# Performance work log

Measured on AMD Instinct MI355X. Metric: run time of the kernel, lower is better.

The kernel has to match this reference:

```python
import math
import jax, jax.numpy as jnp
import numpy as np

B, C, H, W = 64, 1536, 16, 16
M_CLUSTERS, L_DIM, G_DIM, HID = 64, 128, 256, 512


def setup_inputs() -> dict:
    key = jax.random.key(0)
    ks = jax.random.split(key, 10)

    def w(k, out_d, in_d):
        return jax.random.normal(k, (out_d, in_d), jnp.float32) * (1.0 / np.sqrt(in_d))

    return {
        "x": jax.random.normal(ks[0], (B, C, H, W), jnp.float32),
        "t": jax.random.normal(ks[1], (B, C), jnp.float32),
        # token_features: Linear(C,512) -> ReLU -> Linear(512, token_dim)
        "Wt1": w(ks[2], HID, C), "bt1": jnp.zeros((HID,), jnp.float32),
        "Wt2": w(ks[3], G_DIM, HID), "bt2": jnp.zeros((G_DIM,), jnp.float32),
        # cluster_features: Conv1x1(C,512) -> ReLU -> Conv1x1(512, cluster_dim)
        "Wc1": w(ks[4], HID, C), "bc1": jnp.zeros((HID,), jnp.float32),
        "Wc2": w(ks[5], L_DIM, HID), "bc2": jnp.zeros((L_DIM,), jnp.float32),
        # score: Conv1x1(C,512) -> ReLU -> Conv1x1(512, num_clusters)
        "Ws1": w(ks[6], HID, C), "bs1": jnp.zeros((HID,), jnp.float32),
        "Ws2": w(ks[7], M_CLUSTERS, HID), "bs2": jnp.zeros((M_CLUSTERS,), jnp.float32),
        "dust_bin": jnp.float32(1.0),
    }


def _l2norm(a, axis):
    n = jnp.maximum(jnp.linalg.norm(a, axis=axis, keepdims=True), 1e-12)
    return a / n


def _conv1x1_mlp(xf, W1, b1, W2, b2):
    # xf: [B, C, N]; 1x1 convs are channel GEMMs
    h = jax.nn.relu(jnp.einsum('oc,bcn->bon', W1, xf) + b1[None, :, None])
    return jnp.einsum('oc,bcn->bon', W2, h) + b2[None, :, None]


def _matching_probs(S, dust_bin, num_iters=3):
    # Sinkhorn with dustbin row (log domain), reg = 1.0
    b, m, n = S.shape
    dust_row = jnp.broadcast_to(dust_bin.astype(S.dtype), (b, 1, n))
    Ms = jnp.concatenate([S, dust_row], axis=1)  # [B, m+1, n]
    norm = -math.log(n + m)
    log_a = jnp.full((m + 1,), norm, S.dtype).at[-1].add(math.log(n - m))
    log_b = jnp.full((n,), norm, S.dtype)
    u = jnp.zeros((b, m + 1), S.dtype)
    v = jnp.zeros((b, n), S.dtype)
    for _ in range(num_iters):
        u = log_a[None, :] - jax.scipy.special.logsumexp(Ms + v[:, None, :], axis=2)
        v = log_b[None, :] - jax.scipy.special.logsumexp(Ms + u[:, :, None], axis=1)
    return Ms + u[:, :, None] + v[:, None, :] - norm  # log_P - norm


def reference(x, t, Wt1, bt1, Wt2, bt2, Wc1, bc1, Wc2, bc2, Ws1, bs1, Ws2, bs2, dust_bin):
    b, c, h, w = x.shape
    n = h * w
    xf = x.reshape(b, c, n)
    f = _conv1x1_mlp(xf, Wc1, bc1, Wc2, bc2)      # [B, l, N]
    s = _conv1x1_mlp(xf, Ws1, bs1, Ws2, bs2)      # [B, m, N]
    tok = jax.nn.relu(t @ Wt1.T + bt1) @ Wt2.T + bt2  # [B, g]

    log_p = _matching_probs(s, dust_bin, num_iters=3)
    p = jnp.exp(log_p)[:, :-1, :]                 # drop dustbin row -> [B, m, N]

    # (f.unsqueeze(2) * p.unsqueeze(1)).sum(-1) is exactly a batched matmul
    vlad = jnp.einsum('bln,bmn->blm', f, p)       # [B, l, m]
    vlad = _l2norm(vlad, axis=1).reshape(b, -1)   # intra-norm over l, then flatten(1)

    out = jnp.concatenate([_l2norm(tok, axis=-1), vlad], axis=-1)
    return _l2norm(out, axis=-1)
```

## Files before the change

### kernel.cpp

```cpp
#include <hip/hip_runtime.h>
#include <math.h>

#define BNT 16384

using f32x4 = __attribute__((ext_vector_type(4))) float;
using s16x8 = __attribute__((ext_vector_type(8))) short;

__device__ __forceinline__ unsigned short f32_to_bf16_rne(float f) {
  unsigned int u = __float_as_uint(f);
  u += 0x7FFFu + ((u >> 16) & 1u);
  return (unsigned short)(u >> 16);
}
__device__ __forceinline__ unsigned pack_bf16x2(float a, float b) {
  return (unsigned)f32_to_bf16_rne(a) | ((unsigned)f32_to_bf16_rne(b) << 16);
}

__device__ __forceinline__ void gload_lds16(const ushort* g, ushort* lds) {
  __builtin_amdgcn_global_load_lds(
      (const __attribute__((address_space(1))) unsigned int*)g,
      (__attribute__((address_space(3))) unsigned int*)lds, 16, 0, 0);
}

__global__ __launch_bounds__(256) void prep_all(
    const float* __restrict__ t, const float* __restrict__ Wt1,
    const float* __restrict__ Wt2, const float* __restrict__ Wc1,
    const float* __restrict__ Ws1, const float* __restrict__ bc1,
    const float* __restrict__ bs1, const float* __restrict__ Wc2,
    const float* __restrict__ Ws2, const float* __restrict__ bc2,
    const float* __restrict__ bs2, ushort* __restrict__ Tb,
    ushort* __restrict__ Wt1b, ushort* __restrict__ Wt2b,
    ushort* __restrict__ Wc1b, ushort* __restrict__ Ws1b,
    float* __restrict__ b1, ushort* __restrict__ A2, float* __restrict__ b2) {
  const int bid = blockIdx.x, tid = threadIdx.x;
  const float* src = nullptr;
  ushort* dst = nullptr;
  int i = 0;
  if (bid < 96) {
    src = t; dst = Tb; i = bid * 256 + tid;
  } else if (bid < 864) {
    src = Wt1; dst = Wt1b; i = (bid - 96) * 256 + tid;
  } else if (bid < 992) {
    src = Wt2; dst = Wt2b; i = (bid - 864) * 256 + tid;
  } else if (bid < 1760) {
    src = Wc1; dst = Wc1b; i = (bid - 992) * 256 + tid;
  } else if (bid < 2528) {
    src = Ws1; dst = Ws1b; i = (bid - 1760) * 256 + tid;
  } else if (bid < 2532) {
    const int j = (bid - 2528) * 256 + tid;
    b1[j] = j < 512 ? bc1[j] : bs1[j - 512];
    return;
  } else {
    const int r = bid - 2532;
    const int c = tid * 4;
    float v[4] = {0.f, 0.f, 0.f, 0.f};
    if (r < 128) {
      if (c < 512) {
#pragma unroll
        for (int j = 0; j < 4; ++j) v[j] = Wc2[r * 512 + c + j];
      }
    } else if (r < 192) {
      if (c >= 512) {
#pragma unroll
        for (int j = 0; j < 4; ++j) v[j] = Ws2[(r - 128) * 512 + (c - 512) + j];
      }
    }
    uint2 o;
    o.x = pack_bf16x2(v[0], v[1]);
    o.y = pack_bf16x2(v[2], v[3]);
    *(uint2*)(A2 + r * 1024 + c) = o;
    if (tid == 0) b2[r] = r < 128 ? bc2[r] : (r < 192 ? bs2[r - 128] : 0.f);
    return;
  }
  const float4 v = ((const float4*)src)[i];
  uint2 o;
  o.x = pack_bf16x2(v.x, v.y);
  o.y = pack_bf16x2(v.z, v.w);
  ((uint2*)dst)[i] = o;
}

__global__ __launch_bounds__(256) void token1_mfma(
    const ushort* __restrict__ Tb, const ushort* __restrict__ Wt1b,
    float* __restrict__ Pt) {
  const int ct = blockIdx.x, kc = blockIdx.y;
  const int tid = threadIdx.x, l = tid & 63, wv = tid >> 6;
  const int lr = l & 15, ko = l >> 4;
  const int col = ct * 64 + wv * 16 + lr;
  f32x4 acc[4];
#pragma unroll
  for (int r = 0; r < 4; ++r) acc[r] = (f32x4){0.f, 0.f, 0.f, 0.f};
  const int k0 = kc * 384;
#pragma unroll 4
  for (int ks = 0; ks < 12; ++ks) {
    const int k = k0 + ks * 32 + ko * 8;
    const s16x8 bf = *(const s16x8*)(Wt1b + (size_t)col * 1536 + k);
#pragma unroll
    for (int rf = 0; rf < 4; ++rf) {
      const s16x8 af = *(const s16x8*)(Tb + (size_t)(rf * 16 + lr) * 1536 + k);
      acc[rf] =
          __builtin_amdgcn_mfma_f32_16x16x32_bf16(af, bf, acc[rf], 0, 0, 0);
    }
  }
#pragma unroll
  for (int rf = 0; rf < 4; ++rf)
#pragma unroll
    for (int j = 0; j < 4; ++j) {
      const int row = rf * 16 + ko * 4 + j;
      Pt[((kc * 64 + row) << 9) + col] = acc[rf][j];
    }
}

__global__ __launch_bounds__(256) void token1_reduce(
    const float* __restrict__ Pt, const float* __restrict__ bt1,
    ushort* __restrict__ Hb) {
  const int i = blockIdx.x * 256 + threadIdx.x;
  const int row = i >> 8, c2 = (i & 255) * 2;
  float v0 = bt1[c2], v1 = bt1[c2 + 1];
#pragma unroll
  for (int kc = 0; kc < 4; ++kc) {
    v0 += Pt[((kc * 64 + row) << 9) + c2];
    v1 += Pt[((kc * 64 + row) << 9) + c2 + 1];
  }
  v0 = fmaxf(v0, 0.f);
  v1 = fmaxf(v1, 0.f);
  ((unsigned*)Hb)[i] = pack_bf16x2(v0, v1);
}

__global__ __launch_bounds__(256) void token2_mfma(
    const ushort* __restrict__ Hb, const ushort* __restrict__ Wt2b,
    const float* __restrict__ bt2, float* __restrict__ TK) {
  const int ct = blockIdx.x;
  const int tid = threadIdx.x, l = tid & 63, wv = tid >> 6;
  const int lr = l & 15, ko = l >> 4;
  const int col = ct * 64 + wv * 16 + lr;
  f32x4 acc[4];
#pragma unroll
  for (int r = 0; r < 4; ++r) acc[r] = (f32x4){0.f, 0.f, 0.f, 0.f};
#pragma unroll 4
  for (int ks = 0; ks < 16; ++ks) {
    const int k = ks * 32 + ko * 8;
    const s16x8 bf = *(const s16x8*)(Wt2b + (size_t)col * 512 + k);
#pragma unroll
    for (int rf = 0; rf < 4; ++rf) {
      const s16x8 af = *(const s16x8*)(Hb + (size_t)(rf * 16 + lr) * 512 + k);
      acc[rf] =
          __builtin_amdgcn_mfma_f32_16x16x32_bf16(af, bf, acc[rf], 0, 0, 0);
    }
  }
  const float bb = bt2[col];
#pragma unroll
  for (int rf = 0; rf < 4; ++rf)
#pragma unroll
    for (int j = 0; j < 4; ++j)
      TK[(rf * 16 + ko * 4 + j) * 256 + col] = acc[rf][j] + bb;
}

__global__ __launch_bounds__(256) void transpose_x_bf16(
    const float* __restrict__ x, ushort* __restrict__ XT) {
  __shared__ ushort lds[16384];
  const int cc = blockIdx.x * 64, b = blockIdx.y;
  const int t = threadIdx.x;
  const float* xb = x + b * 393216 + cc * 256;
#pragma unroll
  for (int i = 0; i < 16; ++i) {
    const int c0 = i * 4;
    const float v0 = xb[(c0 + 0) * 256 + t];
    const float v1 = xb[(c0 + 1) * 256 + t];
    const float v2 = xb[(c0 + 2) * 256 + t];
    const float v3 = xb[(c0 + 3) * 256 + t];
    uint2 o;
    o.x = pack_bf16x2(v0, v1);
    o.y = pack_bf16x2(v2, v3);
    const int g = c0 >> 3;
    const int waddr = t * 128 + (((g ^ (t & 7)) << 4) | ((c0 & 7) << 1));
    *(uint2*)((char*)lds + waddr) = o;
  }
  __syncthreads();
#pragma unroll
  for (int r = 0; r < 8; ++r) {
    const int j = r * 32 + (t >> 3), q = t & 7;
    const uint4 o =
        *(const uint4*)((const char*)lds + j * 128 + ((q ^ (j & 7)) << 4));
    *(uint4*)(XT + (size_t)(b * 256 + j) * 1536 + cc + q * 8) = o;
  }
}

__global__ __launch_bounds__(512) void gemm1_win(
    const ushort* __restrict__ A1, const ushort* __restrict__ Bt,
    const float* __restrict__ b1, ushort* __restrict__ HT) {
  __shared__ ushort lds[65536];
  const int tid = threadIdx.x, l = tid & 63, w = tid >> 6;
  const int bid = blockIdx.x;
  const int newid = (bid & 7) * 32 + (bid >> 3);
  const int m0 = (newid & 3) * 256, n0 = (newid >> 2) * 256;
  const int wr = w >> 2, wc = w & 3;
  const int lr = l & 15, kq = l >> 4;
  const int permK8 = (kq ^ ((lr >> 1) & 3)) * 8;
  const int aRow = wr * 128 + lr;
  const int bRow = wc * 64 + lr;

  f32x4 acc[8][4];
#pragma unroll
  for (int mi = 0; mi < 8; ++mi)
#pragma unroll
    for (int ni = 0; ni < 4; ++ni) acc[mi][ni] = (f32x4){0.f, 0.f, 0.f, 0.f};

  const int srow = tid >> 2, ssp = tid & 3;
  const int skq = ssp ^ ((srow >> 1) & 3);
  const ushort* sA0 = A1 + (size_t)(m0 + srow) * 1536 + skq * 8;
  const ushort* sA1 = A1 + (size_t)(m0 + srow + 128) * 1536 + skq * 8;
  const ushort* sB0 = Bt + (size_t)(n0 + srow) * 1536 + skq * 8;
  const ushort* sB1 = Bt + (size_t)(n0 + srow + 128) * 1536 + skq * 8;
  const int wofs = w * 512;

#define STG_A(tau, kh)                                              \
  do {                                                              \
    ushort* d = &lds[((((tau)&1) * 2 + (kh)) * 8192) + wofs];       \
    gload_lds16(sA0 + (tau)*64 + (kh)*32, d);                       \
    gload_lds16(sA1 + (tau)*64 + (kh)*32, d + 4096);                \
  } while (0)
#define STG_B(tau, kh)                                              \
  do {                                                              \
    ushort* d = &lds[32768 + ((((tau)&1) * 2 + (kh)) * 8192) + wofs]; \
    gload_lds16(sB0 + (tau)*64 + (kh)*32, d);                       \
    gload_lds16(sB1 + (tau)*64 + (kh)*32, d + 4096);                \
  } while (0)

  STG_A(0, 0);
  STG_B(0, 0);
  STG_A(0, 1);
  STG_B(0, 1);
  asm volatile("s_waitcnt vmcnt(0)" ::: "memory");
  __builtin_amdgcn_s_barrier();

  for (int sg = 0; sg < 24; ++sg) {
    const int rho = sg & 1;
    const int As0 = (rho * 2 + 0) * 8192, As1 = (rho * 2 + 1) * 8192;
    const int Bs0 = 32768 + As0, Bs1 = 32768 + As1;
    const bool st = (sg + 1) < 24;
    s16x8 af[4], bfv[4];

#pragma unroll
    for (int i = 0; i < 4; ++i)
      af[i] = *(const s16x8*)&lds[As0 + (aRow + i * 16) * 32 + permK8];
#pragma unroll
    for (int ni = 0; ni < 4; ++ni)
      bfv[ni] = *(const s16x8*)&lds[Bs0 + (bRow + ni * 16) * 32 + permK8];
    if (st) STG_A(sg + 1, 0);
#pragma unroll
    for (int i = 0; i < 4; ++i)
#pragma unroll
      for (int ni = 0; ni < 4; ++ni)
        acc[i][ni] = __builtin_amdgcn_mfma_f32_16x16x32_bf16(af[i], bfv[ni],
                                                             acc[i][ni], 0, 0, 0);

#pragma unroll
    for (int i = 0; i < 4; ++i)
      af[i] = *(const s16x8*)&lds[As0 + (aRow + 64 + i * 16) * 32 + permK8];
    if (st) STG_B(sg + 1, 0);
#pragma unroll
    for (int i = 0; i < 4; ++i)
#pragma unroll
      for (int ni = 0; ni < 4; ++ni)
        acc[4 + i][ni] = __builtin_amdgcn_mfma_f32_16x16x32_bf16(
            af[i], bfv[ni], acc[4 + i][ni], 0, 0, 0);

#pragma unroll
    for (int i = 0; i < 4; ++i)
      af[i] = *(const s16x8*)&lds[As1 + (aRow + i * 16) * 32 + permK8];
#pragma unroll
    for (int ni = 0; ni < 4; ++ni)
      bfv[ni] = *(const s16x8*)&lds[Bs1 + (bRow + ni * 16) * 32 + permK8];
    if (st) STG_A(sg + 1, 1);
#pragma unroll
    for (int i = 0; i < 4; ++i)
#pragma unroll
      for (int ni = 0; ni < 4; ++ni)
        acc[i][ni] = __builtin_amdgcn_mfma_f32_16x16x32_bf16(af[i], bfv[ni],
                                                             acc[i][ni], 0, 0, 0);

#pragma unroll
    for (int i = 0; i < 4; ++i)
      af[i] = *(const s16x8*)&lds[As1 + (aRow + 64 + i * 16) * 32 + permK8];
    if (st) STG_B(sg + 1, 1);
#pragma unroll
    for (int i = 0; i < 4; ++i)
#pragma unroll
      for (int ni = 0; ni < 4; ++ni)
        acc[4 + i][ni] = __builtin_amdgcn_mfma_f32_16x16x32_bf16(
            af[i], bfv[ni], acc[4 + i][ni], 0, 0, 0);

    if (st) asm volatile("s_waitcnt vmcnt(0)" ::: "memory");
    __builtin_amdgcn_s_barrier();
  }
#undef STG_A
#undef STG_B

#pragma unroll
  for (int mi = 0; mi < 8; ++mi) {
    const int rbase = m0 + wr * 128 + mi * 16 + kq * 4;
    float b4[4];
#pragma unroll
    for (int j = 0; j < 4; ++j) b4[j] = b1[rbase + j];
#pragma unroll
    for (int ni = 0; ni < 4; ++ni) {
      const int col = n0 + wc * 64 + ni * 16 + lr;
      const float v0 = fmaxf(acc[mi][ni][0] + b4[0], 0.f);
      const float v1 = fmaxf(acc[mi][ni][1] + b4[1], 0.f);
      const float v2 = fmaxf(acc[mi][ni][2] + b4[2], 0.f);
      const float v3 = fmaxf(acc[mi][ni][3] + b4[3], 0.f);
      uint2 o;
      o.x = pack_bf16x2(v0, v1);
      o.y = pack_bf16x2(v2, v3);
      *(uint2*)(HT + (size_t)col * 1024 + rbase) = o;
    }
  }
}

__global__ __launch_bounds__(256) void gemm2_mfma96(
    const ushort* __restrict__ A2, const ushort* __restrict__ HT,
    const float* __restrict__ b2, float* __restrict__ C2,
    ushort* __restrict__ Fb) {
  constexpr int K = 1024;
  __shared__ ushort As[2 * 3072];
  __shared__ ushort Bs[2 * 4096];
  const int tid = threadIdx.x;
  const int l = tid & 63, w = tid >> 6;
  const int bid = blockIdx.x;
  const int newid = (bid & 7) * 32 + (bid >> 3);
  const int m0 = (newid & 1) * 96, n0 = (newid >> 1) * 128;
  const int wr = w >> 1, wc = w & 1;
  const int lr = l & 15, kq = l >> 4;

  f32x4 acc[3][4];
#pragma unroll
  for (int mi = 0; mi < 3; ++mi)
#pragma unroll
    for (int ni = 0; ni < 4; ++ni) acc[mi][ni] = (f32x4){0.f, 0.f, 0.f, 0.f};

  const int srow = tid >> 2;
  const int q8 = (tid & 3) * 8;
  const bool secondA = tid < 128;
  const ushort* sA0 = A2 + (size_t)(m0 + srow) * K + q8;
  const ushort* sA1 = A2 + (size_t)(m0 + srow + 64) * K + q8;
  const ushort* sB0 = HT + (size_t)(n0 + srow) * K + q8;
  const ushort* sB1 = HT + (size_t)(n0 + srow + 64) * K + q8;
  const int wofs = w * 512;

#define STAGE2(k0v, buf)                                            \
  do {                                                              \
    gload_lds16(sA0 + (k0v), As + (buf)*3072 + wofs);               \
    if (secondA) gload_lds16(sA1 + (k0v), As + (buf)*3072 + 2048 + wofs); \
    gload_lds16(sB0 + (k0v), Bs + (buf)*4096 + wofs);               \
    gload_lds16(sB1 + (k0v), Bs + (buf)*4096 + 2048 + wofs);        \
  } while (0)

  STAGE2(0, 0);
  __syncthreads();

  int cur = 0;
  for (int k0 = 0; k0 < K; k0 += 32) {
    const int nxt = cur ^ 1;
    if (k0 + 32 < K) STAGE2(k0 + 32, nxt);
    const ushort* Ab = As + cur * 3072;
    const ushort* Bb = Bs + cur * 4096;
    s16x8 af[3], bfr[4];
#pragma unroll
    for (int mi = 0; mi < 3; ++mi)
      af[mi] = *(const s16x8*)(Ab + (wr * 48 + mi * 16 + lr) * 32 + kq * 8);
#pragma unroll
    for (int ni = 0; ni < 4; ++ni)
      bfr[ni] = *(const s16x8*)(Bb + (wc * 64 + ni * 16 + lr) * 32 + kq * 8);
#pragma unroll
    for (int mi = 0; mi < 3; ++mi)
#pragma unroll
      for (int ni = 0; ni < 4; ++ni)
        acc[mi][ni] = __builtin_amdgcn_mfma_f32_16x16x32_bf16(
            af[mi], bfr[ni], acc[mi][ni], 0, 0, 0);
    __syncthreads();
    cur = nxt;
  }
#undef STAGE2

#pragma unroll
  for (int mi = 0; mi < 3; ++mi) {
    const int rbase = m0 + wr * 48 + mi * 16 + kq * 4;
    float b4[4];
#pragma unroll
    for (int j = 0; j < 4; ++j) b4[j] = b2[rbase + j];
    if (rbase < 128) {
#pragma unroll
      for (int ni = 0; ni < 4; ++ni) {
        const int col = n0 + wc * 64 + ni * 16 + lr;
#pragma unroll
        for (int j = 0; j < 4; ++j)
          Fb[(size_t)(rbase + j) * BNT + col] =
              f32_to_bf16_rne(acc[mi][ni][j] + b4[j]);
      }
    } else {
#pragma unroll
      for (int ni = 0; ni < 4; ++ni) {
        const int col = n0 + wc * 64 + ni * 16 + lr;
        float* cr = C2 + (size_t)rbase * BNT + col;
#pragma unroll
        for (int j = 0; j < 4; ++j) cr[(size_t)j * BNT] = acc[mi][ni][j] + b4[j];
      }
    }
  }
}

__global__ __launch_bounds__(256) void sinkhorn_lin(
    const float* __restrict__ S, const float* __restrict__ dustp,
    ushort* __restrict__ Pb) {
  const int b = blockIdx.x, tid = threadIdx.x;
  const int lane = tid & 63, wave = tid >> 6;
  __shared__ float E[65][256];
  __shared__ float U[65];
  __shared__ float V[256];
  for (int idx = tid; idx < 16384; idx += 256) {
    const int m = idx >> 8, n = idx & 255;
    E[m][n] = expf(S[m * BNT + b * 256 + n]);
  }
  E[64][tid] = expf(dustp[0]);
  V[tid] = 1.f;
  const float Ai = 1.f / 320.f;
  const float Adust = 192.f / 320.f;
  const float Bn = 1.f / 320.f;
  __syncthreads();
  for (int it = 0; it < 3; ++it) {
    for (int i = wave; i < 65; i += 4) {
      float s = E[i][lane] * V[lane];
      s = fmaf(E[i][lane + 64], V[lane + 64], s);
      s = fmaf(E[i][lane + 128], V[lane + 128], s);
      s = fmaf(E[i][lane + 192], V[lane + 192], s);
#pragma unroll
      for (int off = 32; off; off >>= 1) s += __shfl_xor(s, off);
      if (lane == 0) U[i] = (i == 64 ? Adust : Ai) / s;
    }
    __syncthreads();
    {
      const int n = tid;
      float s = 0.f;
#pragma unroll 13
      for (int i = 0; i < 65; ++i) s = fmaf(E[i][n], U[i], s);
      V[n] = Bn / s;
    }
    __syncthreads();
  }
  for (int idx = tid; idx < 16384; idx += 256) {
    const int m = idx >> 8, n = idx & 255;
    Pb[b * 16384 + idx] = f32_to_bf16_rne(E[m][n] * U[m] * V[n] * 320.f);
  }
}

__global__ __launch_bounds__(256) void vlad_mfma(const ushort* __restrict__ Fb,
                                                 const ushort* __restrict__ Pb,
                                                 float* __restrict__ VL) {
  const int b = blockIdx.x;
  const int tid = threadIdx.x, l = tid & 63, w = tid >> 6;
  const int lr = l & 15, ko = l >> 4;
  f32x4 acc[2][4];
#pragma unroll
  for (int li = 0; li < 2; ++li)
#pragma unroll
    for (int ni = 0; ni < 4; ++ni) acc[li][ni] = (f32x4){0.f, 0.f, 0.f, 0.f};
  const ushort* Fbase = Fb + b * 256;
  const ushort* Pbase = Pb + b * 16384;
#pragma unroll
  for (int ks = 0; ks < 8; ++ks) {
    const int k = ks * 32 + ko * 8;
    s16x8 bfr[4];
#pragma unroll
    for (int ni = 0; ni < 4; ++ni)
      bfr[ni] = *(const s16x8*)(Pbase + (ni * 16 + lr) * 256 + k);
#pragma unroll
    for (int li = 0; li < 2; ++li) {
      const s16x8 af =
          *(const s16x8*)(Fbase + (size_t)(w * 32 + li * 16 + lr) * BNT + k);
#pragma unroll
      for (int ni = 0; ni < 4; ++ni)
        acc[li][ni] = __builtin_amdgcn_mfma_f32_16x16x32_bf16(
            af, bfr[ni], acc[li][ni], 0, 0, 0);
    }
  }
#pragma unroll
  for (int li = 0; li < 2; ++li)
#pragma unroll
    for (int ni = 0; ni < 4; ++ni)
#pragma unroll
      for (int j = 0; j < 4; ++j) {
        const int ll = w * 32 + li * 16 + ko * 4 + j;
        const int m = ni * 16 + lr;
        VL[b * 8192 + ll * 64 + m] = acc[li][ni][j];
      }
}

__global__ __launch_bounds__(256) void finalize_kernel(
    const float* __restrict__ TK, const float* __restrict__ VL,
    float* __restrict__ out) {
  const int b = blockIdx.x, tid = threadIdx.x;
  const int lane = tid & 63, wave = tid >> 6;
  __shared__ float sred[4];
  __shared__ float ssm_part[4][64];
  __shared__ float invm_s[64];
  __shared__ float totals[1];
  const float* vl = &VL[b * 8192];
  float accv = 0.f;
  for (int k = 0; k < 32; ++k) {
    const float xv = vl[tid + 256 * k];
    accv = fmaf(xv, xv, accv);
  }
  ssm_part[wave][lane] = accv;
  const float tv = TK[b * 256 + tid];
  float ss = tv * tv;
#pragma unroll
  for (int off = 32; off; off >>= 1) ss += __shfl_down(ss, off);
  if (lane == 0) sred[wave] = ss;
  __syncthreads();
  const float sstok = sred[0] + sred[1] + sred[2] + sred[3];
  const float invtok = 1.f / fmaxf(sqrtf(sstok), 1e-12f);
  float tpart = 0.f;
  if (wave == 0) {
    const float s4 = ssm_part[0][tid] + ssm_part[1][tid] + ssm_part[2][tid] +
                     ssm_part[3][tid];
    const float inv = 1.f / fmaxf(sqrtf(s4), 1e-12f);
    invm_s[tid] = inv;
    tpart = s4 * inv * inv;
#pragma unroll
    for (int off = 32; off; off >>= 1) tpart += __shfl_down(tpart, off);
    if (lane == 0) totals[0] = tpart;
  }
  __syncthreads();
  const float total = totals[0] + sstok * invtok * invtok;
  const float invT = 1.f / fmaxf(sqrtf(total), 1e-12f);
  float* ob = &out[b * 8448];
  ob[tid] = tv * invtok * invT;
  for (int k = 0; k < 32; ++k) {
    const int idx = tid + 256 * k;
    ob[256 + idx] = vl[idx] * invm_s[idx & 63] * invT;
  }
}

template <bool RELU>
__global__ __launch_bounds__(256) void gemm_tt(
    const float* __restrict__ A, const float* __restrict__ Bw,
    const float* __restrict__ bias, float* __restrict__ C, int K, int Nn) {
  __shared__ float As[16][68];
  __shared__ float Bs[16][68];
  const int tid = threadIdx.x;
  const int tx = tid & 15, ty = tid >> 4;
  const int n0 = blockIdx.x * 64;
  const int lrow = tid >> 2, lkq = (tid & 3) << 2;
  float acc[4][4];
#pragma unroll
  for (int r = 0; r < 4; ++r)
#pragma unroll
    for (int c = 0; c < 4; ++c) acc[r][c] = 0.f;
  for (int k0 = 0; k0 < K; k0 += 16) {
    const float4 av = *(const float4*)&A[lrow * K + k0 + lkq];
    const float4 bv = *(const float4*)&Bw[(n0 + lrow) * K + k0 + lkq];
    As[lkq + 0][lrow] = av.x;
    As[lkq + 1][lrow] = av.y;
    As[lkq + 2][lrow] = av.z;
    As[lkq + 3][lrow] = av.w;
    Bs[lkq + 0][lrow] = bv.x;
    Bs[lkq + 1][lrow] = bv.y;
    Bs[lkq + 2][lrow] = bv.z;
    Bs[lkq + 3][lrow] = bv.w;
    __syncthreads();
#pragma unroll
    for (int kk = 0; kk < 16; ++kk) {
      const float4 a4 = *(const float4*)&As[kk][ty << 2];
      const float4 b4 = *(const float4*)&Bs[kk][tx << 2];
      acc[0][0] = fmaf(a4.x, b4.x, acc[0][0]);
      acc[0][1] = fmaf(a4.x, b4.y, acc[0][1]);
      acc[0][2] = fmaf(a4.x, b4.z, acc[0][2]);
      acc[0][3] = fmaf(a4.x, b4.w, acc[0][3]);
      acc[1][0] = fmaf(a4.y, b4.x, acc[1][0]);
      acc[1][1] = fmaf(a4.y, b4.y, acc[1][1]);
      acc[1][2] = fmaf(a4.y, b4.z, acc[1][2]);
      acc[1][3] = fmaf(a4.y, b4.w, acc[1][3]);
      acc[2][0] = fmaf(a4.z, b4.x, acc[2][0]);
      acc[2][1] = fmaf(a4.z, b4.y, acc[2][1]);
      acc[2][2] = fmaf(a4.z, b4.z, acc[2][2]);
      acc[2][3] = fmaf(a4.z, b4.w, acc[2][3]);
      acc[3][0] = fmaf(a4.w, b4.x, acc[3][0]);
      acc[3][1] = fmaf(a4.w, b4.y, acc[3][1]);
      acc[3][2] = fmaf(a4.w, b4.z, acc[3][2]);
      acc[3][3] = fmaf(a4.w, b4.w, acc[3][3]);
    }
    __syncthreads();
  }
#pragma unroll
  for (int r = 0; r < 4; ++r) {
    const int row = (ty << 2) + r;
    float4 o;
    o.x = acc[r][0] + bias[n0 + (tx << 2) + 0];
    o.y = acc[r][1] + bias[n0 + (tx << 2) + 1];
    o.z = acc[r][2] + bias[n0 + (tx << 2) + 2];
    o.w = acc[r][3] + bias[n0 + (tx << 2) + 3];
    if (RELU) {
      o.x = fmaxf(o.x, 0.f);
      o.y = fmaxf(o.y, 0.f);
      o.z = fmaxf(o.z, 0.f);
      o.w = fmaxf(o.w, 0.f);
    }
    *(float4*)&C[row * Nn + n0 + (tx << 2)] = o;
  }
}

template <bool XVIEW, bool RELU>
__global__ __launch_bounds__(256) void gemm_tile(
    const float* __restrict__ A, const float* __restrict__ Bsrc,
    const float* __restrict__ bias, float* __restrict__ Cout, int K) {
  __shared__ float As[16][68];
  __shared__ float Bsh[16][68];
  const int tid = threadIdx.x;
  const int tx = tid & 15, ty = tid >> 4;
  const int rowBase = blockIdx.y * 64;
  const int colBase = blockIdx.x * 64;
  const int bb = colBase >> 8, n0 = colBase & 255;
  const int boff = XVIEW ? (bb * 393216 + n0) : colBase;
  const int la_row = tid >> 2, la_kq = (tid & 3) << 2;
  const int lb_k = tid >> 4, lb_c = (tid & 15) << 2;
  float acc[4][4];
#pragma unroll
  for (int r = 0; r < 4; ++r)
#pragma unroll
    for (int c = 0; c < 4; ++c) acc[r][c] = 0.f;
  for (int k0 = 0; k0 < K; k0 += 16) {
    const float4 av = *(const float4*)&A[(rowBase + la_row) * K + k0 + la_kq];
    float4 bv;
    if (XVIEW)
      bv = *(const float4*)&Bsrc[boff + (k0 + lb_k) * 256 + lb_c];
    else
      bv = *(const float4*)&Bsrc[(k0 + lb_k) * BNT + boff + lb_c];
    As[la_kq + 0][la_row] = av.x;
    As[la_kq + 1][la_row] = av.y;
    As[la_kq + 2][la_row] = av.z;
    As[la_kq + 3][la_row] = av.w;
    *(float4*)&Bsh[lb_k][lb_c] = bv;
    __syncthreads();
#pragma unroll
    for (int kk = 0; kk < 16; ++kk) {
      const float4 a4 = *(const float4*)&As[kk][ty << 2];
      const float4 b4 = *(const float4*)&Bsh[kk][tx << 2];
      acc[0][0] = fmaf(a4.x, b4.x, acc[0][0]);
      acc[0][1] = fmaf(a4.x, b4.y, acc[0][1]);
      acc[0][2] = fmaf(a4.x, b4.z, acc[0][2]);
      acc[0][3] = fmaf(a4.x, b4.w, acc[0][3]);
      acc[1][0] = fmaf(a4.y, b4.x, acc[1][0]);
      acc[1][1] = fmaf(a4.y, b4.y, acc[1][1]);
      acc[1][2] = fmaf(a4.y, b4.z, acc[1][2]);
      acc[1][3] = fmaf(a4.y, b4.w, acc[1][3]);
      acc[2][0] = fmaf(a4.z, b4.x, acc[2][0]);
      acc[2][1] = fmaf(a4.z, b4.y, acc[2][1]);
      acc[2][2] = fmaf(a4.z, b4.z, acc[2][2]);
      acc[2][3] = fmaf(a4.z, b4.w, acc[2][3]);
      acc[3][0] = fmaf(a4.w, b4.x, acc[3][0]);
      acc[3][1] = fmaf(a4.w, b4.y, acc[3][1]);
      acc[3][2] = fmaf(a4.w, b4.z, acc[3][2]);
      acc[3][3] = fmaf(a4.w, b4.w, acc[3][3]);
    }
    __syncthreads();
  }
#pragma unroll
  for (int r = 0; r < 4; ++r) {
    const int row = rowBase + (ty << 2) + r;
    const float bsv = bias[row];
    float4 o;
    o.x = acc[r][0] + bsv;
    o.y = acc[r][1] + bsv;
    o.z = acc[r][2] + bsv;
    o.w = acc[r][3] + bsv;
    if (RELU) {
      o.x = fmaxf(o.x, 0.f);
      o.y = fmaxf(o.y, 0.f);
      o.z = fmaxf(o.z, 0.f);
      o.w = fmaxf(o.w, 0.f);
    }
    *(float4*)&Cout[row * BNT + colBase + (tx << 2)] = o;
  }
}

__global__ __launch_bounds__(256) void sinkhorn_kernel(
    const float* __restrict__ S, const float* __restrict__ dustp,
    float* __restrict__ P) {
  const int b = blockIdx.x, tid = threadIdx.x;
  const int lane = tid & 63, wave = tid >> 6;
  __shared__ float Ms[65][256];
  __shared__ float u[65];
  __shared__ float v[256];
  const float dust = dustp[0];
  for (int idx = tid; idx < 16384; idx += 256) {
    const int m = idx >> 8, n = idx & 255;
    Ms[m][n] = S[m * BNT + b * 256 + n];
  }
  Ms[64][tid] = dust;
  v[tid] = 0.f;
  if (tid < 65) u[tid] = 0.f;
  const float norm = -logf(320.f);
  const float la_dust = norm + logf(192.f);
  __syncthreads();
  for (int it = 0; it < 3; ++it) {
    for (int i = wave; i < 65; i += 4) {
      const float x0 = Ms[i][lane] + v[lane];
      const float x1 = Ms[i][lane + 64] + v[lane + 64];
      const float x2 = Ms[i][lane + 128] + v[lane + 128];
      const float x3 = Ms[i][lane + 192] + v[lane + 192];
      float mm = fmaxf(fmaxf(x0, x1), fmaxf(x2, x3));
#pragma unroll
      for (int off = 32; off; off >>= 1) mm = fmaxf(mm, __shfl_xor(mm, off));
      float s = expf(x0 - mm) + expf(x1 - mm) + expf(x2 - mm) + expf(x3 - mm);
#pragma unroll
      for (int off = 32; off; off >>= 1) s += __shfl_xor(s, off);
      if (lane == 0) u[i] = (i == 64 ? la_dust : norm) - (logf(s) + mm);
    }
    __syncthreads();
    {
      const int n = tid;
      float mm = -1e30f;
      for (int i = 0; i < 65; ++i) mm = fmaxf(mm, Ms[i][n] + u[i]);
      float s = 0.f;
      for (int i = 0; i < 65; ++i) s += expf(Ms[i][n] + u[i] - mm);
      v[n] = norm - (logf(s) + mm);
    }
    __syncthreads();
  }
  for (int idx = tid; idx < 16384; idx += 256) {
    const int m = idx >> 8, n = idx & 255;
    P[b * 16384 + idx] = expf(Ms[m][n] + u[m] + v[n] - norm);
  }
}

__device__ __forceinline__ int ps_idx(int m, int n) {
  return m * 256 + ((((n >> 2) ^ (m & 7)) << 2) | (n & 3));
}
__global__ __launch_bounds__(256) void vlad_kernel(const float* __restrict__ F,
                                                   const float* __restrict__ P,
                                                   float* __restrict__ VL) {
  const int b = blockIdx.x, half = blockIdx.y;
  const int tid = threadIdx.x;
  const int m = tid & 63, lg = tid >> 6;
  __shared__ float ps[64 * 256];
  for (int idx = tid; idx < 16384; idx += 256) {
    const int mm = idx >> 8, n = idx & 255;
    ps[ps_idx(mm, n)] = P[b * 16384 + idx];
  }
  __syncthreads();
  float acc[16];
#pragma unroll
  for (int i = 0; i < 16; ++i) acc[i] = 0.f;
  for (int i = 0; i < 16; ++i) {
    const int ll = half * 64 + lg + 4 * i;
    const float* frow = &F[(size_t)ll * BNT + b * 256];
    float a = 0.f;
#pragma unroll 8
    for (int nq = 0; nq < 64; ++nq) {
      const float4 f4 = *(const float4*)&frow[nq << 2];
      const float4 p4 = *(const float4*)&ps[m * 256 + ((nq ^ (m & 7)) << 2)];
      a = fmaf(f4.x, p4.x, a);
      a = fmaf(f4.y, p4.y, a);
      a = fmaf(f4.z, p4.z, a);
      a = fmaf(f4.w, p4.w, a);
    }
    acc[i] = a;
  }
#pragma unroll
  for (int i = 0; i < 16; ++i) {
    const int ll = half * 64 + lg + 4 * i;
    VL[b * 8192 + ll * 64 + m] = acc[i];
  }
}

extern "C" void kernel_launch(void* const* d_in, const int* in_sizes, int n_in,
                              void* d_out, int out_size, void* d_ws,
                              size_t ws_size, hipStream_t stream) {
  const float* x = (const float*)d_in[0];
  const float* t = (const float*)d_in[1];
  const float* Wt1 = (const float*)d_in[2];
  const float* bt1 = (const float*)d_in[3];
  const float* Wt2 = (const float*)d_in[4];
  const float* bt2 = (const float*)d_in[5];
  const float* Wc1 = (const float*)d_in[6];
  const float* bc1 = (const float*)d_in[7];
  const float* Wc2 = (const float*)d_in[8];
  const float* bc2 = (const float*)d_in[9];
  const float* Ws1 = (const float*)d_in[10];
  const float* bs1 = (const float*)d_in[11];
  const float* Ws2 = (const float*)d_in[12];
  const float* bs2 = (const float*)d_in[13];
  const float* dust = (const float*)d_in[14];
  float* out = (float*)d_out;

  if (ws_size >= 97714176ull) {
    char* base = (char*)d_ws;
    ushort* Tb = (ushort*)base;
    ushort* Wt1b = (ushort*)(base + 196608);
    ushort* Wt2b = (ushort*)(base + 1769472);
    float* Pt = (float*)(base + 2031616);
    ushort* Hb = (ushort*)(base + 2555904);
    ushort* XT = (ushort*)base;
    ushort* Pb = (ushort*)base;
    float* VL = (float*)(base + 4194304);
    ushort* Fb = (ushort*)(base + 8388608);
    ushort* HT = (ushort*)(base + 50331648);
    float* C2 = (float*)(base + 83886080);
    ushort* A1 = (ushort*)(base + 83886080);
    ushort* Wc1b = A1;
    ushort* Ws1b = (ushort*)(base + 85458944);
    ushort* A2 = (ushort*)(base + 96468992);
    float* b2 = (float*)(base + 96993280);
    float* TK = (float*)(base + 96994304);
    float* b1 = (float*)(base + 97059840);
    float* Sb = C2 + (size_t)128 * BNT;

    prep_all<<<2788, 256, 0, stream>>>(t, Wt1, Wt2, Wc1, Ws1, bc1, bs1, Wc2,
                                       Ws2, bc2, bs2, Tb, Wt1b, Wt2b, Wc1b,
                                       Ws1b, b1, A2, b2);
    token1_mfma<<<dim3(8, 4), 256, 0, stream>>>(Tb, Wt1b, Pt);
    token1_reduce<<<64, 256, 0, stream>>>(Pt, bt1, Hb);
    token2_mfma<<<4, 256, 0, stream>>>(Hb, Wt2b, bt2, TK);
    transpose_x_bf16<<<dim3(24, 64), 256, 0, stream>>>(x, XT);
    gemm1_win<<<256, 512, 0, stream>>>(A1, XT, b1, HT);
    gemm2_mfma96<<<256, 256, 0, stream>>>(A2, HT, b2, C2, Fb);
    sinkhorn_lin<<<64, 256, 0, stream>>>(Sb, dust, Pb);
    vlad_mfma<<<64, 256, 0, stream>>>(Fb, Pb, VL);
    finalize_kernel<<<64, 256, 0, stream>>>(TK, VL, out);
  } else {
    float* ws = (float*)d_ws;
    float* H = ws;
    float* F = H + 512 * BNT;
    float* Sb = F + 128 * BNT;
    float* P = Sb + 64 * BNT;
    float* VL = P + 64 * BNT;
    float* TK = VL + 64 * 8192;
    float* Hh = P;

    gemm_tt<true><<<dim3(8, 1), 256, 0, stream>>>(t, Wt1, bt1, Hh, 1536, 512);
    gemm_tt<false><<<dim3(4, 1), 256, 0, stream>>>(Hh, Wt2, bt2, TK, 512, 256);
    gemm_tile<true, true><<<dim3(256, 8), 256, 0, stream>>>(Wc1, x, bc1, H, 1536);
    gemm_tile<false, false><<<dim3(256, 2), 256, 0, stream>>>(Wc2, H, bc2, F, 512);
    gemm_tile<true, true><<<dim3(256, 8), 256, 0, stream>>>(Ws1, x, bs1, H, 1536);
    gemm_tile<false, false><<<dim3(256, 1), 256, 0, stream>>>(Ws2, H, bs2, Sb, 512);
    sinkhorn_kernel<<<64, 256, 0, stream>>>(Sb, dust, P);
    vlad_kernel<<<dim3(64, 2), 256, 0, stream>>>(F, P, VL);
    finalize_kernel<<<64, 256, 0, stream>>>(TK, VL, out);
  }
}
```

Baseline: 166.1 us.

## Fuse sinkhorn, vlad and finalize into one kernel; add 8-phase gemm1 schedule

Sinkhorn, the VLAD matmul and the final normalization now run as one per-batch kernel. P is kept in swizzled LDS as bf16 and VLAD results are reused in LDS, so two launches and the global round-trips of P and VL are removed. Separately, the main gemm1 loop gets extra barriers around each MFMA cluster, s_setprio raising, and partial vmcnt waits instead of a full drain. The extra barriers add sync cost, and the 64-block post kernel's large LDS footprint limits occupancy.

```diff
diff --git a/kernel.cpp b/kernel.cpp
--- a/kernel.cpp
+++ b/kernel.cpp
@@ -184,7 +184,7 @@
   }
 }
 
-__global__ __launch_bounds__(512) void gemm1_win(
+__global__ __launch_bounds__(512) void gemm1_8ph(
     const ushort* __restrict__ A1, const ushort* __restrict__ Bt,
     const float* __restrict__ b1, ushort* __restrict__ HT) {
   __shared__ ushort lds[65536];
@@ -246,23 +246,35 @@
     for (int ni = 0; ni < 4; ++ni)
       bfv[ni] = *(const s16x8*)&lds[Bs0 + (bRow + ni * 16) * 32 + permK8];
     if (st) STG_A(sg + 1, 0);
+    __builtin_amdgcn_s_barrier();
+    __builtin_amdgcn_s_setprio(1);
 #pragma unroll
     for (int i = 0; i < 4; ++i)
 #pragma unroll
       for (int ni = 0; ni < 4; ++ni)
         acc[i][ni] = __builtin_amdgcn_mfma_f32_16x16x32_bf16(af[i], bfv[ni],
                                                              acc[i][ni], 0, 0, 0);
+    __builtin_amdgcn_s_setprio(0);
+    __builtin_amdgcn_s_barrier();
 
 #pragma unroll
     for (int i = 0; i < 4; ++i)
       af[i] = *(const s16x8*)&lds[As0 + (aRow + 64 + i * 16) * 32 + permK8];
     if (st) STG_B(sg + 1, 0);
+    if (sg < 23)
+      asm volatile("s_waitcnt vmcnt(4)" ::: "memory");
+    else
+      asm volatile("s_waitcnt vmcnt(0)" ::: "memory");
+    __builtin_amdgcn_s_barrier();
+    __builtin_amdgcn_s_setprio(1);
 #pragma unroll
     for (int i = 0; i < 4; ++i)
 #pragma unroll
       for (int ni = 0; ni < 4; ++ni)
         acc[4 + i][ni] = __builtin_amdgcn_mfma_f32_16x16x32_bf16(
             af[i], bfv[ni], acc[4 + i][ni], 0, 0, 0);
+    __builtin_amdgcn_s_setprio(0);
+    __builtin_amdgcn_s_barrier();
 
 #pragma unroll
     for (int i = 0; i < 4; ++i)
@@ -271,25 +283,31 @@
     for (int ni = 0; ni < 4; ++ni)
       bfv[ni] = *(const s16x8*)&lds[Bs1 + (bRow + ni * 16) * 32 + permK8];
     if (st) STG_A(sg + 1, 1);
+    __builtin_amdgcn_s_barrier();
+    __builtin_amdgcn_s_setprio(1);
 #pragma unroll
     for (int i = 0; i < 4; ++i)
 #pragma unroll
       for (int ni = 0; ni < 4; ++ni)
         acc[i][ni] = __builtin_amdgcn_mfma_f32_16x16x32_bf16(af[i], bfv[ni],
                                                              acc[i][ni], 0, 0, 0);
+    __builtin_amdgcn_s_setprio(0);
+    __builtin_amdgcn_s_barrier();
 
 #pragma unroll
     for (int i = 0; i < 4; ++i)
       af[i] = *(const s16x8*)&lds[As1 + (aRow + 64 + i * 16) * 32 + permK8];
     if (st) STG_B(sg + 1, 1);
+    asm volatile("s_waitcnt vmcnt(4)" ::: "memory");
+    __builtin_amdgcn_s_barrier();
+    __builtin_amdgcn_s_setprio(1);
 #pragma unroll
     for (int i = 0; i < 4; ++i)
 #pragma unroll
       for (int ni = 0; ni < 4; ++ni)
         acc[4 + i][ni] = __builtin_amdgcn_mfma_f32_16x16x32_bf16(
             af[i], bfv[ni], acc[4 + i][ni], 0, 0, 0);
-
-    if (st) asm volatile("s_waitcnt vmcnt(0)" ::: "memory");
+    __builtin_amdgcn_s_setprio(0);
     __builtin_amdgcn_s_barrier();
   }
 #undef STG_A
@@ -408,14 +426,24 @@
   }
 }
 
-__global__ __launch_bounds__(256) void sinkhorn_lin(
+__global__ __launch_bounds__(256) void post_kernel(
     const float* __restrict__ S, const float* __restrict__ dustp,
-    ushort* __restrict__ Pb) {
+    const ushort* __restrict__ Fb, const float* __restrict__ TK,
+    float* __restrict__ out) {
+  __shared__ char smem[100672];
+  float(*E)[256] = (float(*)[256])smem;
+  float* U = (float*)(smem + 66560);
+  float* V = (float*)(smem + 66880);
+  ushort* Pl = (ushort*)(smem + 67904);
+  float* VLs = (float*)smem;
+  float* sred = (float*)(smem + 32768);
+  float* ssm = (float*)(smem + 32784);
+  float* invm_s = (float*)(smem + 33808);
+  float* totals = (float*)(smem + 34064);
+
   const int b = blockIdx.x, tid = threadIdx.x;
   const int lane = tid & 63, wave = tid >> 6;
-  __shared__ float E[65][256];
-  __shared__ float U[65];
-  __shared__ float V[256];
+
   for (int idx = tid; idx < 16384; idx += 256) {
     const int m = idx >> 8, n = idx & 255;
     E[m][n] = expf(S[m * BNT + b * 256 + n]);
@@ -446,17 +474,25 @@
     }
     __syncthreads();
   }
-  for (int idx = tid; idx < 16384; idx += 256) {
-    const int m = idx >> 8, n = idx & 255;
-    Pb[b * 16384 + idx] = f32_to_bf16_rne(E[m][n] * U[m] * V[n] * 320.f);
-  }
-}
-
-__global__ __launch_bounds__(256) void vlad_mfma(const ushort* __restrict__ Fb,
-                                                 const ushort* __restrict__ Pb,
-                                                 float* __restrict__ VL) {
-  const int b = blockIdx.x;
-  const int tid = threadIdx.x, l = tid & 63, w = tid >> 6;
+#pragma unroll
+  for (int j = 0; j < 8; ++j) {
+    const int gg = tid + j * 256;
+    const int row = gg >> 5, gr = gg & 31;
+    const float um = U[row];
+    const int n0g = gr * 8;
+    float p[8];
+#pragma unroll
+    for (int e = 0; e < 8; ++e)
+      p[e] = E[row][n0g + e] * um * V[n0g + e] * 320.f;
+    uint4 o;
+    o.x = pack_bf16x2(p[0], p[1]);
+    o.y = pack_bf16x2(p[2], p[3]);
+    o.z = pack_bf16x2(p[4], p[5]);
+    o.w = pack_bf16x2(p[6], p[7]);
+    *(uint4*)(Pl + row * 256 + ((gr ^ (row & 7)) << 3)) = o;
+  }
+  __syncthreads();
+  const int l = lane, w = wave;
   const int lr = l & 15, ko = l >> 4;
   f32x4 acc[2][4];
 #pragma unroll
@@ -464,14 +500,16 @@
 #pragma unroll
     for (int ni = 0; ni < 4; ++ni) acc[li][ni] = (f32x4){0.f, 0.f, 0.f, 0.f};
   const ushort* Fbase = Fb + b * 256;
-  const ushort* Pbase = Pb + b * 16384;
 #pragma unroll
   for (int ks = 0; ks < 8; ++ks) {
+    s16x8 bfr[4];
+#pragma unroll
+    for (int ni = 0; ni < 4; ++ni) {
+      const int row = ni * 16 + lr;
+      const int gk = ks * 4 + ko;
+      bfr[ni] = *(const s16x8*)(Pl + row * 256 + ((gk ^ (row & 7)) << 3));
+    }
     const int k = ks * 32 + ko * 8;
-    s16x8 bfr[4];
-#pragma unroll
-    for (int ni = 0; ni < 4; ++ni)
-      bfr[ni] = *(const s16x8*)(Pbase + (ni * 16 + lr) * 256 + k);
 #pragma unroll
     for (int li = 0; li < 2; ++li) {
       const s16x8 af =
@@ -490,8 +528,43 @@
       for (int j = 0; j < 4; ++j) {
         const int ll = w * 32 + li * 16 + ko * 4 + j;
         const int m = ni * 16 + lr;
-        VL[b * 8192 + ll * 64 + m] = acc[li][ni][j];
+        VLs[ll * 64 + m] = acc[li][ni][j];
       }
+  __syncthreads();
+  float accv = 0.f;
+  for (int k = 0; k < 32; ++k) {
+    const float xv = VLs[tid + 256 * k];
+    accv = fmaf(xv, xv, accv);
+  }
+  ssm[wave * 64 + lane] = accv;
+  const float tv = TK[b * 256 + tid];
+  float ss = tv * tv;
+#pragma unroll
+  for (int off = 32; off; off >>= 1) ss += __shfl_down(ss, off);
+  if (lane == 0) sred[wave] = ss;
+  __syncthreads();
+  const float sstok = sred[0] + sred[1] + sred[2] + sred[3];
+  const float invtok = 1.f / fmaxf(sqrtf(sstok), 1e-12f);
+  float tpart = 0.f;
+  if (wave == 0) {
+    const float s4 =
+        ssm[tid] + ssm[64 + tid] + ssm[128 + tid] + ssm[192 + tid];
+    const float inv = 1.f / fmaxf(sqrtf(s4), 1e-12f);
+    invm_s[tid] = inv;
+    tpart = s4 * inv * inv;
+#pragma unroll
+    for (int off = 32; off; off >>= 1) tpart += __shfl_down(tpart, off);
+    if (lane == 0) totals[0] = tpart;
+  }
+  __syncthreads();
+  const float total = totals[0] + sstok * invtok * invtok;
+  const float invT = 1.f / fmaxf(sqrtf(total), 1e-12f);
+  float* ob = &out[b * 8448];
+  ob[tid] = tv * invtok * invT;
+  for (int k = 0; k < 32; ++k) {
+    const int idx = tid + 256 * k;
+    ob[256 + idx] = VLs[idx] * invm_s[idx & 63] * invT;
+  }
 }
 
 __global__ __launch_bounds__(256) void finalize_kernel(
@@ -800,8 +873,6 @@
     float* Pt = (float*)(base + 2031616);
     ushort* Hb = (ushort*)(base + 2555904);
     ushort* XT = (ushort*)base;
-    ushort* Pb = (ushort*)base;
-    float* VL = (float*)(base + 4194304);
     ushort* Fb = (ushort*)(base + 8388608);
     ushort* HT = (ushort*)(base + 50331648);
     float* C2 = (float*)(base + 83886080);
@@ -821,11 +892,9 @@
     token1_reduce<<<64, 256, 0, stream>>>(Pt, bt1, Hb);
     token2_mfma<<<4, 256, 0, stream>>>(Hb, Wt2b, bt2, TK);
     transpose_x_bf16<<<dim3(24, 64), 256, 0, stream>>>(x, XT);
-    gemm1_win<<<256, 512, 0, stream>>>(A1, XT, b1, HT);
+    gemm1_8ph<<<256, 512, 0, stream>>>(A1, XT, b1, HT);
     gemm2_mfma96<<<256, 256, 0, stream>>>(A2, HT, b2, C2, Fb);
-    sinkhorn_lin<<<64, 256, 0, stream>>>(Sb, dust, Pb);
-    vlad_mfma<<<64, 256, 0, stream>>>(Fb, Pb, VL);
-    finalize_kernel<<<64, 256, 0, stream>>>(TK, VL, out);
+    post_kernel<<<64, 256, 0, stream>>>(Sb, dust, Fb, TK, out);
   } else {
     float* ws = (float*)d_ws;
     float* H = ws;
```

Result: faster. 159.2 us (-4.2%).
